# Kernel tuning notes

Hardware: AMD Instinct MI355X
Metric: run time of the kernel (lower is better)

## Reference

```python
import jax, jax.numpy as jnp
import numpy as np
import math

B, S, D, H = 2, 2048, 1024, 16
DK = D // H


def setup_inputs() -> dict:
    key = jax.random.key(0)
    ks = jax.random.split(key, 11)
    s = 1.0 / math.sqrt(D)
    return {
        "q": jax.random.normal(ks[0], (B, S, D), jnp.float32),
        "k": jax.random.normal(ks[1], (B, S, D), jnp.float32),
        "v": jax.random.normal(ks[2], (B, S, D), jnp.float32),
        "Wq": jax.random.normal(ks[3], (D, D), jnp.float32) * s,
        "bq": jax.random.normal(ks[4], (D,), jnp.float32) * s,
        "Wk": jax.random.normal(ks[5], (D, D), jnp.float32) * s,
        "bk": jax.random.normal(ks[6], (D,), jnp.float32) * s,
        "Wv": jax.random.normal(ks[7], (D, D), jnp.float32) * s,
        "bv": jax.random.normal(ks[8], (D,), jnp.float32) * s,
        "Wo": jax.random.normal(ks[9], (D, D), jnp.float32) * s,
        "bo": jax.random.normal(ks[10], (D,), jnp.float32) * s,
    }


def reference(q, k, v, Wq, bq, Wk, bk, Wv, bv, Wo, bo):
    bs = q.shape[0]
    # linear projections, split heads: [B, H, S, DK]
    qh = (q @ Wq.T + bq).reshape(bs, -1, H, DK).transpose(0, 2, 1, 3)
    kh = (k @ Wk.T + bk).reshape(bs, -1, H, DK).transpose(0, 2, 1, 3)
    vh = (v @ Wv.T + bv).reshape(bs, -1, H, DK).transpose(0, 2, 1, 3)
    # scaled dot-product attention (dropout in eval mode -> identity)
    scores = jnp.einsum('bhqd,bhkd->bhqk', qh, kh) / math.sqrt(DK)
    attn = jax.nn.softmax(scores, axis=-1)
    out = jnp.einsum('bhqk,bhkd->bhqd', attn, vh)
    concat = out.transpose(0, 2, 1, 3).reshape(bs, -1, D)
    return concat @ Wo.T + bo
```

## Files before the change

### kernel.cpp

```cpp
#include <hip/hip_runtime.h>
#include <stdint.h>

#define DEV __device__ __forceinline__

typedef __bf16 bf16;
typedef __bf16 bf16x8 __attribute__((ext_vector_type(8)));
typedef unsigned short u16x8 __attribute__((ext_vector_type(8)));
typedef unsigned short u16x4 __attribute__((ext_vector_type(4)));
typedef float f32x4 __attribute__((ext_vector_type(4)));
typedef uint32_t u32x4 __attribute__((ext_vector_type(4)));

static constexpr int S = 2048, D = 1024, NH = 16;
static constexpr float QSCALE = 0.125f * 1.44269504088896340736f;
static constexpr float STHR = 4096.0f;

union BU { u16x8 u; bf16x8 v; };
union PU { u32x4 u; bf16x8 v; };

DEV uint32_t pack2(float a, float b) {
  union { __bf16 h; uint16_t u; } x, y;
  x.h = (__bf16)a; y.h = (__bf16)b;
  return (uint32_t)x.u | ((uint32_t)y.u << 16);
}

struct CvtArgs { const float* s[7]; bf16* d[7]; };
__global__ __launch_bounds__(256) void cvt_all(CvtArgs a) {
  int blk = blockIdx.x, seg, rel;
  if (blk < 6144) { seg = blk >> 11; rel = blk & 2047; }
  else { int bb = blk - 6144; seg = 3 + (bb >> 9); rel = bb & 511; }
  int i = rel * 256 + threadIdx.x;
  const float4* p = (const float4*)a.s[seg] + (size_t)i * 2;
  float4 x = p[0], y = p[1];
  bf16x8 o;
  o[0] = (bf16)x.x; o[1] = (bf16)x.y; o[2] = (bf16)x.z; o[3] = (bf16)x.w;
  o[4] = (bf16)y.x; o[5] = (bf16)y.y; o[6] = (bf16)y.z; o[7] = (bf16)y.w;
  ((bf16x8*)a.d[seg])[i] = o;
}

DEV void async_copy16(bf16* lds_dst, const bf16* g_src) {
  __builtin_amdgcn_global_load_lds(
      (const __attribute__((address_space(1))) void*)(g_src),
      (__attribute__((address_space(3))) void*)(lds_dst),
      16, 0, 0);
}

struct GArgs {
  const bf16* A[3]; const bf16* W[3]; const float* bias[3];
  bf16* Cb[3]; float scale[3];
};

__global__ __launch_bounds__(256, 2)
void gemm128(GArgs g) {
  constexpr int N = 1024, K = 1024;
  const int z = blockIdx.z;
  const bf16* A = g.A[z];
  const bf16* Bt = g.W[z];
  const float* bias = g.bias[z];
  const float scale = g.scale[z];

  __shared__ bf16 As[128 * 32];
  __shared__ bf16 Bs[128 * 32];
  const int t = threadIdx.x;
  const int w = t >> 6, l = t & 63;
  const int wr = w >> 1, wc = w & 1;
  const int lr = l & 15, lg = l >> 4;
  const int m0 = blockIdx.y * 128, n0 = blockIdx.x * 128;

  f32x4 acc[4][4] = {};

  const int srow = t >> 2, scol = (t & 3) * 8;
  const bf16* Aptr = A + (size_t)(m0 + srow) * K + scol;
  const bf16* Bptr = Bt + (size_t)(n0 + srow) * K + scol;
  bf16* AsDst = &As[w * 512];
  bf16* BsDst = &Bs[w * 512];

  for (int k0 = 0; k0 < K; k0 += 32) {
    async_copy16(AsDst,        Aptr + k0);
    async_copy16(AsDst + 2048, Aptr + (size_t)64 * K + k0);
    async_copy16(BsDst,        Bptr + k0);
    async_copy16(BsDst + 2048, Bptr + (size_t)64 * K + k0);
    __syncthreads();
    bf16x8 af[4], bfr[4];
#pragma unroll
    for (int i = 0; i < 4; i++)
      af[i] = *(const bf16x8*)&As[(wr * 64 + i * 16 + lr) * 32 + lg * 8];
#pragma unroll
    for (int i = 0; i < 4; i++)
      bfr[i] = *(const bf16x8*)&Bs[(wc * 64 + i * 16 + lr) * 32 + lg * 8];
#pragma unroll
    for (int mi = 0; mi < 4; mi++)
#pragma unroll
      for (int ni = 0; ni < 4; ni++)
        acc[mi][ni] = __builtin_amdgcn_mfma_f32_16x16x32_bf16(
            af[mi], bfr[ni], acc[mi][ni], 0, 0, 0);
    __syncthreads();
  }

#pragma unroll
  for (int mi = 0; mi < 4; mi++) {
#pragma unroll
    for (int ni = 0; ni < 4; ni++) {
      int col = n0 + wc * 64 + ni * 16 + lr;
      float bv = bias[col];
#pragma unroll
      for (int r = 0; r < 4; r++) {
        int row = m0 + wr * 64 + mi * 16 + lg * 4 + r;
        g.Cb[z][(size_t)row * N + col] = (bf16)((acc[mi][ni][r] + bv) * scale);
      }
    }
  }
}

__global__ __launch_bounds__(256, 2)
void gemm64out(const bf16* __restrict__ A, const bf16* __restrict__ Bt,
               const float* __restrict__ bias, float* __restrict__ Cf) {
  constexpr int N = 1024, K = 1024;
  __shared__ bf16 As[128 * 32];
  __shared__ bf16 Bs[64 * 32];
  const int t = threadIdx.x;
  const int w = t >> 6, l = t & 63;
  const int lr = l & 15, lg = l >> 4;
  const int m0 = blockIdx.y * 128, n0 = blockIdx.x * 64;

  f32x4 acc[2][4] = {};

  const int srow = t >> 2, scol = (t & 3) * 8;
  const bf16* Aptr = A + (size_t)(m0 + srow) * K + scol;
  const bf16* Bptr = Bt + (size_t)(n0 + srow) * K + scol;
  bf16* AsDst = &As[w * 512];
  bf16* BsDst = &Bs[w * 512];

  for (int k0 = 0; k0 < K; k0 += 32) {
    async_copy16(AsDst,        Aptr + k0);
    async_copy16(AsDst + 2048, Aptr + (size_t)64 * K + k0);
    async_copy16(BsDst,        Bptr + k0);
    __syncthreads();
    bf16x8 af[2], bfr[4];
#pragma unroll
    for (int i = 0; i < 2; i++)
      af[i] = *(const bf16x8*)&As[(w * 32 + i * 16 + lr) * 32 + lg * 8];
#pragma unroll
    for (int n = 0; n < 4; n++)
      bfr[n] = *(const bf16x8*)&Bs[(n * 16 + lr) * 32 + lg * 8];
#pragma unroll
    for (int mi = 0; mi < 2; mi++)
#pragma unroll
      for (int ni = 0; ni < 4; ni++)
        acc[mi][ni] = __builtin_amdgcn_mfma_f32_16x16x32_bf16(
            af[mi], bfr[ni], acc[mi][ni], 0, 0, 0);
    __syncthreads();
  }

#pragma unroll
  for (int mi = 0; mi < 2; mi++) {
#pragma unroll
    for (int ni = 0; ni < 4; ni++) {
      int col = n0 + ni * 16 + lr;
      float bv = bias[col];
#pragma unroll
      for (int r = 0; r < 4; r++) {
        int row = m0 + w * 32 + mi * 16 + lg * 4 + r;
        Cf[(size_t)row * N + col] = acc[mi][ni][r] + bv;
      }
    }
  }
}

__global__ __launch_bounds__(512, 4)
void attn_kernel(const bf16* __restrict__ Qp, const bf16* __restrict__ Kp,
                 const bf16* __restrict__ Vp, bf16* __restrict__ Oc) {
  __shared__ uint4 ldsu[2048];
  char* lds = (char*)ldsu;

  const int t = threadIdx.x, w = t >> 6, l = t & 63;
  const int lr = l & 15, lg = l >> 4;
  const int bh = blockIdx.y, b = bh >> 4, h = bh & 15;
  const int q0 = blockIdx.x * 128;
  const size_t base = (size_t)b * S * D + (size_t)h * 64;
  const size_t TILE = (size_t)64 * D;

  bf16x8 qf[2];
  {
    const bf16* qrow = Qp + base + (size_t)(q0 + w * 16 + lr) * D + lg * 8;
    qf[0] = *(const bf16x8*)(qrow);
    qf[1] = *(const bf16x8*)(qrow + 32);
  }

  f32x4 accO[4] = {};
  float mrun = 4.0f, lsum = 0.f;

  const bf16* kptr;
  {
    int o = t * 16;
    int rho = o >> 7;
    int seg16 = ((o & 127) ^ ((rho & 7) << 4)) >> 4;
    int mm = rho >> 4;
    int srow = ((mm & 1) << 5) | (((rho >> 2) & 3) << 3) | ((mm >> 1) << 2) | (rho & 3);
    kptr = Kp + base + (size_t)srow * D + seg16 * 8;
  }
  bf16* kdst = (bf16*)(lds + w * 1024);

  const int vu = t & 31, vcc = t >> 5;
  const bf16* Vg = Vp + base + (size_t)(2 * vu) * D + vcc * 4;
  int vwa[4];
#pragma unroll
  for (int j = 0; j < 4; j++) {
    int d = vcc * 4 + j;
    vwa[j] = 16384 + ((d * 128 + vu * 4) ^ ((d & 7) << 4));
  }

  const int rswz = (lr & 7) << 4;

  async_copy16(kdst, kptr);
  u16x4 va = *(const u16x4*)(Vg);
  u16x4 vb = *(const u16x4*)(Vg + D);
  __syncthreads();
#pragma unroll
  for (int j = 0; j < 4; j++)
    *(uint32_t*)(lds + vwa[j]) = (uint32_t)va[j] | ((uint32_t)vb[j] << 16);
  va = *(const u16x4*)(Vg + TILE);
  vb = *(const u16x4*)(Vg + TILE + D);
  __syncthreads();

  const bf16* kp1 = kptr + TILE;
  const bf16* vg2 = Vg + 2 * TILE;

#pragma unroll 2
  for (int it = 0; it < 32; ++it) {
    const int cur = (it & 1) * 8192;
    const int nxt = ((it + 1) & 1) * 8192;
    const bool hasN = it < 31, hasN2 = it < 30;

    if (hasN) {
      async_copy16((bf16*)(lds + nxt + w * 1024), kp1);
      kp1 += TILE;
    }
    const bf16* pv = hasN2 ? vg2 : (Vp + base);
    u16x4 ta = *(const u16x4*)(pv);
    u16x4 tb = *(const u16x4*)(pv + D);
    vg2 += TILE;

    f32x4 sc[4] = {};
#pragma unroll
    for (int ks = 0; ks < 2; ks++) {
      BU kf[4];
#pragma unroll
      for (int m = 0; m < 4; m++)
        kf[m].u = *(const u16x8*)(lds + cur +
                   ((((m * 16 + lr) * 128) + ks * 64 + lg * 16) ^ rswz));
      __builtin_amdgcn_s_setprio(1);
#pragma unroll
      for (int m = 0; m < 4; m++)
        sc[m] = __builtin_amdgcn_mfma_f32_16x16x32_bf16(
            kf[m].v, qf[ks], sc[m], 0, 0, 0);
      __builtin_amdgcn_s_setprio(0);
    }

    float s = 0.f;
#pragma unroll
    for (int m = 0; m < 4; m++) {
      sc[m][0] = exp2f(sc[m][0] - mrun);
      sc[m][1] = exp2f(sc[m][1] - mrun);
      sc[m][2] = exp2f(sc[m][2] - mrun);
      sc[m][3] = exp2f(sc[m][3] - mrun);
      s += (sc[m][0] + sc[m][1]) + (sc[m][2] + sc[m][3]);
    }
    if (!__all(s <= STHR)) {
      float pm = sc[0][0];
#pragma unroll
      for (int m = 0; m < 4; m++)
#pragma unroll
        for (int r = 0; r < 4; r++) pm = fmaxf(pm, sc[m][r]);
      pm = fmaxf(pm, __shfl_xor(pm, 16));
      pm = fmaxf(pm, __shfl_xor(pm, 32));
      float mn = fmaxf(mrun + __log2f(pm), mrun);
      float f = exp2f(mrun - mn);
      mrun = mn;
      s *= f;
      lsum *= f;
#pragma unroll
      for (int m = 0; m < 4; m++)
#pragma unroll
        for (int r = 0; r < 4; r++) sc[m][r] *= f;
#pragma unroll
      for (int r = 0; r < 4; r++) {
        float a = __shfl(f, (lg << 4) | (lg * 4 + r));
#pragma unroll
        for (int n = 0; n < 4; n++) accO[n][r] *= a;
      }
    }
    lsum += s;
    uint32_t pk[4][2];
#pragma unroll
    for (int m = 0; m < 4; m++) {
      pk[m][0] = pack2(sc[m][0], sc[m][1]);
      pk[m][1] = pack2(sc[m][2], sc[m][3]);
    }

    if (hasN) {
#pragma unroll
      for (int j = 0; j < 4; j++)
        *(uint32_t*)(lds + vwa[j] + nxt) = (uint32_t)va[j] | ((uint32_t)vb[j] << 16);
    }

#pragma unroll
    for (int ks = 0; ks < 2; ks++) {
      PU pa;
      pa.u[0] = pk[ks][0];
      pa.u[1] = pk[ks][1];
      pa.u[2] = pk[2 + ks][0];
      pa.u[3] = pk[2 + ks][1];
      BU vf[4];
#pragma unroll
      for (int n = 0; n < 4; n++)
        vf[n].u = *(const u16x8*)(lds + 16384 + cur +
                   ((((n * 16 + lr) * 128) + ks * 64 + lg * 16) ^ rswz));
      __builtin_amdgcn_s_setprio(1);
#pragma unroll
      for (int n = 0; n < 4; n++)
        accO[n] = __builtin_amdgcn_mfma_f32_16x16x32_bf16(
            pa.v, vf[n].v, accO[n], 0, 0, 0);
      __builtin_amdgcn_s_setprio(0);
    }

    va = ta; vb = tb;
    __syncthreads();
  }

  lsum += __shfl_xor(lsum, 16);
  lsum += __shfl_xor(lsum, 32);
#pragma unroll
  for (int r = 0; r < 4; r++) {
    float lv = __shfl(lsum, (lg << 4) | (lg * 4 + r));
    float rl = 1.0f / lv;
    int row = q0 + w * 16 + lg * 4 + r;
    bf16* orow = Oc + base + (size_t)row * D;
#pragma unroll
    for (int n = 0; n < 4; n++) orow[n * 16 + lr] = (bf16)(accO[n][r] * rl);
  }
}

extern "C" void kernel_launch(void* const* d_in, const int* in_sizes, int n_in,
                              void* d_out, int out_size, void* d_ws, size_t ws_size,
                              hipStream_t stream) {
  const float* q  = (const float*)d_in[0];
  const float* k  = (const float*)d_in[1];
  const float* v  = (const float*)d_in[2];
  const float* Wq = (const float*)d_in[3];
  const float* bq = (const float*)d_in[4];
  const float* Wk = (const float*)d_in[5];
  const float* bk = (const float*)d_in[6];
  const float* Wv = (const float*)d_in[7];
  const float* bv = (const float*)d_in[8];
  const float* Wo = (const float*)d_in[9];
  const float* bo = (const float*)d_in[10];
  float* out = (float*)d_out;

  const int BS = 2 * S;
  const size_t SZ_T = (size_t)BS * D * 2;
  const size_t SZ_W = (size_t)D * D * 2;

  char* ws = (char*)d_ws;
  bf16* qb  = (bf16*)(ws);
  bf16* kb  = (bf16*)(ws + SZ_T);
  bf16* vb  = (bf16*)(ws + 2 * SZ_T);
  bf16* Wqb = (bf16*)(ws + 3 * SZ_T);
  bf16* Wkb = (bf16*)(ws + 3 * SZ_T + SZ_W);
  bf16* Wvb = (bf16*)(ws + 3 * SZ_T + 2 * SZ_W);
  bf16* Wob = (bf16*)(ws + 3 * SZ_T + 3 * SZ_W);
  bf16* Qh  = (bf16*)(ws + 3 * SZ_T + 4 * SZ_W);
  bf16* Kh  = (bf16*)(ws + 4 * SZ_T + 4 * SZ_W);
  bf16* Vh  = (bf16*)(ws + 5 * SZ_T + 4 * SZ_W);
  bf16* Oc  = qb;

  CvtArgs ca;
  ca.s[0] = q;  ca.d[0] = qb;
  ca.s[1] = k;  ca.d[1] = kb;
  ca.s[2] = v;  ca.d[2] = vb;
  ca.s[3] = Wq; ca.d[3] = Wqb;
  ca.s[4] = Wk; ca.d[4] = Wkb;
  ca.s[5] = Wv; ca.d[5] = Wvb;
  ca.s[6] = Wo; ca.d[6] = Wob;
  cvt_all<<<dim3(8192), 256, 0, stream>>>(ca);

  GArgs gp = {};
  gp.A[0] = qb; gp.W[0] = Wqb; gp.bias[0] = bq; gp.Cb[0] = Qh; gp.scale[0] = QSCALE;
  gp.A[1] = kb; gp.W[1] = Wkb; gp.bias[1] = bk; gp.Cb[1] = Kh; gp.scale[1] = 1.0f;
  gp.A[2] = vb; gp.W[2] = Wvb; gp.bias[2] = bv; gp.Cb[2] = Vh; gp.scale[2] = 1.0f;
  gemm128<<<dim3(D / 128, BS / 128, 3), 256, 0, stream>>>(gp);

  attn_kernel<<<dim3(S / 128, 2 * NH), 512, 0, stream>>>(Qh, Kh, Vh, Oc);

  gemm64out<<<dim3(D / 64, BS / 128), 256, 0, stream>>>(Oc, Wob, bo, out);
}
```

Baseline: 237.0 us.

## Use hardware bf16 pack/exp2 intrinsics and remap block order for XCD locality

Replaces the software float-to-bf16 conversions with the v_cvt_pk_bf16_f32 instruction in the cast kernel, GEMM epilogues and attention output. Swaps exp2f for the raw hardware exp2 builtin in the softmax. Remaps block indices in both GEMMs and the attention kernel so that consecutive tiles land on the same XCD, which should improve L2 reuse. The raw exp2 skips denormal/range handling, and the remap assumes the grid dimensions are exact multiples of the swizzle factor.

After: 214.7 us. -9.4%, faster.

```diff
diff --git a/kernel.cpp b/kernel.cpp
--- a/kernel.cpp
+++ b/kernel.cpp
@@ -17,10 +17,12 @@
 union BU { u16x8 u; bf16x8 v; };
 union PU { u32x4 u; bf16x8 v; };
 
+DEV float fexp2(float x) { return __builtin_amdgcn_exp2f(x); }
+
 DEV uint32_t pack2(float a, float b) {
-  union { __bf16 h; uint16_t u; } x, y;
-  x.h = (__bf16)a; y.h = (__bf16)b;
-  return (uint32_t)x.u | ((uint32_t)y.u << 16);
+  uint32_t r;
+  asm("v_cvt_pk_bf16_f32 %0, %1, %2" : "=v"(r) : "v"(a), "v"(b));
+  return r;
 }
 
 struct CvtArgs { const float* s[7]; bf16* d[7]; };
@@ -31,10 +33,12 @@
   int i = rel * 256 + threadIdx.x;
   const float4* p = (const float4*)a.s[seg] + (size_t)i * 2;
   float4 x = p[0], y = p[1];
-  bf16x8 o;
-  o[0] = (bf16)x.x; o[1] = (bf16)x.y; o[2] = (bf16)x.z; o[3] = (bf16)x.w;
-  o[4] = (bf16)y.x; o[5] = (bf16)y.y; o[6] = (bf16)y.z; o[7] = (bf16)y.w;
-  ((bf16x8*)a.d[seg])[i] = o;
+  u32x4 o;
+  o[0] = pack2(x.x, x.y);
+  o[1] = pack2(x.z, x.w);
+  o[2] = pack2(y.x, y.y);
+  o[3] = pack2(y.z, y.w);
+  ((u32x4*)a.d[seg])[i] = o;
 }
 
 DEV void async_copy16(bf16* lds_dst, const bf16* g_src) {
@@ -64,7 +68,9 @@
   const int w = t >> 6, l = t & 63;
   const int wr = w >> 1, wc = w & 1;
   const int lr = l & 15, lg = l >> 4;
-  const int m0 = blockIdx.y * 128, n0 = blockIdx.x * 128;
+  const int orig = blockIdx.x + (blockIdx.y << 3);
+  const int tl = ((orig & 7) << 5) | (orig >> 3);
+  const int m0 = (tl >> 3) * 128, n0 = (tl & 7) * 128;
 
   f32x4 acc[4][4] = {};
 
@@ -105,7 +111,8 @@
 #pragma unroll
       for (int r = 0; r < 4; r++) {
         int row = m0 + wr * 64 + mi * 16 + lg * 4 + r;
-        g.Cb[z][(size_t)row * N + col] = (bf16)((acc[mi][ni][r] + bv) * scale);
+        uint32_t pk = pack2((acc[mi][ni][r] + bv) * scale, 0.f);
+        *(uint16_t*)&g.Cb[z][(size_t)row * N + col] = (uint16_t)pk;
       }
     }
   }
@@ -120,7 +127,9 @@
   const int t = threadIdx.x;
   const int w = t >> 6, l = t & 63;
   const int lr = l & 15, lg = l >> 4;
-  const int m0 = blockIdx.y * 128, n0 = blockIdx.x * 64;
+  const int orig = blockIdx.x + (blockIdx.y << 4);
+  const int tl = ((orig & 7) << 6) | (orig >> 3);
+  const int m0 = (tl >> 4) * 128, n0 = (tl & 15) * 64;
 
   f32x4 acc[2][4] = {};
 
@@ -174,8 +183,11 @@
 
   const int t = threadIdx.x, w = t >> 6, l = t & 63;
   const int lr = l & 15, lg = l >> 4;
-  const int bh = blockIdx.y, b = bh >> 4, h = bh & 15;
-  const int q0 = blockIdx.x * 128;
+  const int orig = blockIdx.x + (blockIdx.y << 4);
+  const int tl = ((orig & 7) << 6) | (orig >> 3);
+  const int qblk = tl & 15, bh = tl >> 4;
+  const int b = bh >> 4, h = bh & 15;
+  const int q0 = qblk * 128;
   const size_t base = (size_t)b * S * D + (size_t)h * 64;
   const size_t TILE = (size_t)64 * D;
 
@@ -259,10 +271,10 @@
     float s = 0.f;
 #pragma unroll
     for (int m = 0; m < 4; m++) {
-      sc[m][0] = exp2f(sc[m][0] - mrun);
-      sc[m][1] = exp2f(sc[m][1] - mrun);
-      sc[m][2] = exp2f(sc[m][2] - mrun);
-      sc[m][3] = exp2f(sc[m][3] - mrun);
+      sc[m][0] = fexp2(sc[m][0] - mrun);
+      sc[m][1] = fexp2(sc[m][1] - mrun);
+      sc[m][2] = fexp2(sc[m][2] - mrun);
+      sc[m][3] = fexp2(sc[m][3] - mrun);
       s += (sc[m][0] + sc[m][1]) + (sc[m][2] + sc[m][3]);
     }
     if (!__all(s <= STHR)) {
@@ -274,7 +286,7 @@
       pm = fmaxf(pm, __shfl_xor(pm, 16));
       pm = fmaxf(pm, __shfl_xor(pm, 32));
       float mn = fmaxf(mrun + __log2f(pm), mrun);
-      float f = exp2f(mrun - mn);
+      float f = fexp2(mrun - mn);
       mrun = mn;
       s *= f;
       lsum *= f;
@@ -336,7 +348,10 @@
     int row = q0 + w * 16 + lg * 4 + r;
     bf16* orow = Oc + base + (size_t)row * D;
 #pragma unroll
-    for (int n = 0; n < 4; n++) orow[n * 16 + lr] = (bf16)(accO[n][r] * rl);
+    for (int n = 0; n < 4; n++) {
+      uint32_t pkv = pack2(accO[n][r] * rl, 0.f);
+      *(uint16_t*)&orow[n * 16 + lr] = (uint16_t)pkv;
+    }
   }
 }
 
```
